# Kernel tuning notes

Measured on AMD Instinct MI355X. Metric: run time of the kernel, lower is better.

The kernel has to match this reference:

```python
import jax, jax.numpy as jnp
import numpy as np

N_WIN, P, K, PAD, M_SEL, B_SZ, C, DH = 2048, 64, 48, 8, 1536, 8, 128, 32
INNER = (C * 4 * 2 // 3 // 32) * 32  # gated GLU inner dim = 320


def _ln(x, g, b, eps=1e-5):
    m = x.mean(-1, keepdims=True)
    v = ((x - m) ** 2).mean(-1, keepdims=True)
    return (x - m) * jax.lax.rsqrt(v + eps) * g + b


def _forward(x, n1_g, n1_b, n2_g, n2_b, qkv_w, qkv_b, proj_w, proj_b,
             ls1_g, ls2_g, glu_w, glu_b, out_w, out_b,
             index_window, index_token, padding_index, asy_index, M, B, enable_CB):
    N, P_, C_ = x.shape
    H = C_ // DH
    scale = DH ** -0.5
    x = _ln(x, n1_g, n1_b)                              # norm1
    X = x                                               # (N, P, C) normalized copy
    XX = x[index_window].reshape(-1, C_)                # (M*P, C) gathered windows
    xn = XX.at[asy_index].set(_ln(XX[asy_index], n2_g, n2_b))
    shortcut = xn[asy_index]
    xt = xn[index_token].reshape(M, -1, C_)             # (M, K, C)
    Kt = xt.shape[1]
    qkv = (xt @ qkv_w + qkv_b).reshape(M, Kt, H, 3 * DH).transpose(0, 2, 1, 3)
    q, k, v = jnp.split(qkv, 3, axis=3)                 # each (M, H, K, DH)
    attn = jnp.einsum('mhqd,mhkd->mhqk', q, k) * scale  # (M, H, K, K)
    # scatter scores into dense per-token map keyed by KEY position, mask pads, gather back
    attn_map = jnp.zeros((XX.shape[0], Kt, H), attn.dtype)
    attn_map = attn_map.at[index_token].set(jnp.transpose(attn, (0, 3, 2, 1)).reshape(-1, Kt, H))
    attn_map = attn_map.at[padding_index].set(-10000.0)
    attn = jnp.transpose(attn_map[index_token].reshape(M, Kt, Kt, H), (0, 3, 2, 1))
    attn = jax.nn.softmax(attn, axis=-1)
    o = jnp.einsum('mhqk,mhkd->mqhd', attn, v).reshape(M, Kt, C_)
    o = o @ proj_w + proj_b
    XX = XX.at[index_token].set(o.reshape(-1, C_))
    xa = XX[asy_index]
    # sub-layers: ls1 -> residual -> norm2 -> mlp(+CB) -> ls2 -> residual
    xa = shortcut + xa * ls1_g
    shortcut = xa
    xa = _ln(xa, n2_g, n2_b)
    u, g = jnp.split(xa @ glu_w + glu_b, 2, axis=-1)
    xa = (u * jax.nn.gelu(g, approximate=False)) @ out_w + out_b
    if enable_CB:
        tXX = jnp.zeros_like(XX).at[asy_index].set(xa)
        tX = jnp.zeros_like(X).at[index_window].set(tXX.reshape(M, -1, C_))
        tX = tX.reshape(B, -1, C_)
        tX = 0.5 * tX + 0.5 * tX.mean(axis=1, keepdims=True)
        xa = tX.reshape(N, P_, C_)[index_window].reshape(-1, C_)[asy_index]
    xa = shortcut + xa * ls2_g
    XX = XX.at[asy_index].set(xa)
    XX = XX.at[padding_index].set(X[index_window].reshape(-1, C_)[padding_index])
    return X.at[index_window].set(XX.reshape(M, -1, C_))  # (N, P, C)


def setup_inputs() -> dict:
    key = jax.random.key(0)
    ks = jax.random.split(key, 6)
    rng = np.random.default_rng(0)
    index_window = jnp.asarray(np.sort(rng.choice(N_WIN, M_SEL, replace=False)).astype(np.int64))
    base = np.arange(M_SEL)[:, None] * P + np.arange(K)[None, :]   # (M, K) flat token ids in [0, M*P)
    pad = np.zeros((M_SEL, K), dtype=bool)
    pad[:, K - PAD:] = True                                        # last PAD tokens of each window are padding
    index_token = jnp.asarray(base.reshape(-1).astype(np.int64))   # (M*K,)
    padding_index = jnp.asarray(base[pad].astype(np.int64))        # (M*PAD,)
    asy_index = jnp.asarray(base[~pad].astype(np.int64))           # (M*(K-PAD),)
    s = 0.02
    return {
        'x': jax.random.normal(ks[0], (N_WIN, P, C), jnp.float32),
        'n1_g': jnp.ones((C,), jnp.float32), 'n1_b': jnp.zeros((C,), jnp.float32),
        'n2_g': jnp.ones((C,), jnp.float32), 'n2_b': jnp.zeros((C,), jnp.float32),
        'qkv_w': jax.random.normal(ks[1], (C, 3 * C), jnp.float32) * s,
        'qkv_b': jnp.zeros((3 * C,), jnp.float32),
        'proj_w': jax.random.normal(ks[2], (C, C), jnp.float32) * s,
        'proj_b': jnp.zeros((C,), jnp.float32),
        'ls1_g': jnp.full((C,), 1e-5, jnp.float32), 'ls2_g': jnp.full((C,), 1e-5, jnp.float32),
        'glu_w': jax.random.normal(ks[3], (C, 2 * INNER), jnp.float32) * s,
        'glu_b': jnp.zeros((2 * INNER,), jnp.float32),
        'out_w': jax.random.normal(ks[4], (INNER, C), jnp.float32) * s,
        'out_b': jnp.zeros((C,), jnp.float32),
        'index_window': index_window, 'index_token': index_token,
        'padding_index': padding_index, 'asy_index': asy_index,
        'M': M_SEL, 'B': B_SZ, 'enable_CB': 1,
    }


def reference(x, n1_g, n1_b, n2_g, n2_b, qkv_w, qkv_b, proj_w, proj_b,
              ls1_g, ls2_g, glu_w, glu_b, out_w, out_b,
              index_window, index_token, padding_index, asy_index, M, B, enable_CB):
    return _forward(x, n1_g, n1_b, n2_g, n2_b, qkv_w, qkv_b, proj_w, proj_b,
                    ls1_g, ls2_g, glu_w, glu_b, out_w, out_b,
                    index_window, index_token, padding_index, asy_index, M, B, enable_CB)
```

## Files before the change

### kernel.cpp

```cpp
#include <hip/hip_runtime.h>
#include <math.h>

typedef unsigned short u16;
typedef unsigned int   u32;
typedef __attribute__((ext_vector_type(8))) short bf16x8;
typedef __attribute__((ext_vector_type(4))) float f32x4;

#define N_WIN 2048
#define PW    64
#define KA    40
#define MSEL  1536
#define CH    128
#define NH    4
#define GLUI  320
#define NTOK  (MSEL*KA)
#define RPC   16384

__device__ __forceinline__ u16 f2b(float f) {
    u32 u = __float_as_uint(f);
    return (u16)((u + 0x7FFFu + ((u >> 16) & 1u)) >> 16);
}
__device__ __forceinline__ float b2f(u16 v) { return __uint_as_float(((u32)v) << 16); }

__device__ __forceinline__ float fgelu(float g) {
    return g / (1.f + __expf(-1.702f * g));
}

__global__ __launch_bounds__(256) void k_cvt(const float* __restrict__ qkv_w,
                                             const float* __restrict__ proj_w,
                                             const float* __restrict__ glu_w,
                                             const float* __restrict__ out_w,
                                             const int* __restrict__ iw,
                                             u16* __restrict__ wq, u16* __restrict__ wp,
                                             u16* __restrict__ wg, u16* __restrict__ wo,
                                             float* __restrict__ csum,
                                             int* __restrict__ selidx) {
    int idx = blockIdx.x * 256 + threadIdx.x;
    if (idx < 49152) {
        int n = idx / 128, k = idx % 128;
        wq[idx] = f2b(qkv_w[k * 384 + n]);
    } else if (idx < 65536) {
        int i = idx - 49152, n = i / 128, k = i % 128;
        wp[i] = f2b(proj_w[k * 128 + n]);
    } else if (idx < 147456) {
        int i = idx - 65536, n = i / 128, k = i % 128;
        wg[i] = f2b(glu_w[k * 640 + n]);
    } else if (idx < 188416) {
        int i = idx - 147456, n = i / 320, k = i % 320;
        wo[i] = f2b(out_w[k * 128 + n]);
    } else if (idx < 188416 + 8 * CH) {
        csum[idx - 188416] = 0.f;
    } else if (idx < 188416 + 8 * CH + N_WIN) {
        int w_ = idx - (188416 + 8 * CH);
        int lo = 0, hi = MSEL - 1, m = -1;
        while (lo <= hi) {
            int mid = (lo + hi) >> 1;
            int vw = iw[mid];
            if (vw == w_) { m = mid; break; }
            if (vw < w_) lo = mid + 1; else hi = mid - 1;
        }
        selidx[w_] = m;
    }
}

__global__ __launch_bounds__(256) void k_ln1(const float* __restrict__ x,
                                             const float* __restrict__ g1,
                                             const float* __restrict__ b1,
                                             const float* __restrict__ g2,
                                             const float* __restrict__ b2,
                                             const int* __restrict__ selidx,
                                             float* __restrict__ out,
                                             u16* __restrict__ s1h) {
    int wave = threadIdx.x >> 6, lane = threadIdx.x & 63;
    long row = (long)blockIdx.x * 8 + wave * 2 + (lane >> 5);
    int col = (lane & 31) * 4;
    float4 v = *(const float4*)(x + row * CH + col);
    float s  = v.x + v.y + v.z + v.w;
    float s2 = v.x * v.x + v.y * v.y + v.z * v.z + v.w * v.w;
    #pragma unroll
    for (int o = 16; o; o >>= 1) { s += __shfl_xor(s, o); s2 += __shfl_xor(s2, o); }
    float mu = s * (1.f / CH), var = s2 * (1.f / CH) - mu * mu;
    float r = rsqrtf(var + 1e-5f);
    float4 gg = *(const float4*)(g1 + col);
    float4 bb = *(const float4*)(b1 + col);
    f32x4 o4;
    o4[0] = (v.x - mu) * r * gg.x + bb.x;
    o4[1] = (v.y - mu) * r * gg.y + bb.y;
    o4[2] = (v.z - mu) * r * gg.z + bb.z;
    o4[3] = (v.w - mu) * r * gg.w + bb.w;

    int w_ = (int)(row >> 6), k_ = (int)(row & 63);
    int m = selidx[w_];
    bool overwritten = (m >= 0) && (k_ < KA);
    if (!overwritten) {
        __builtin_nontemporal_store(o4, (f32x4*)(out + row * CH + col));
    } else {
        float t  = o4[0] + o4[1] + o4[2] + o4[3];
        float t2 = o4[0] * o4[0] + o4[1] * o4[1] + o4[2] * o4[2] + o4[3] * o4[3];
        #pragma unroll
        for (int o = 16; o; o >>= 1) { t += __shfl_xor(t, o); t2 += __shfl_xor(t2, o); }
        float mu2 = t * (1.f / CH), var2 = t2 * (1.f / CH) - mu2 * mu2;
        float r2 = rsqrtf(var2 + 1e-5f);
        float4 gg2 = *(const float4*)(g2 + col);
        float4 bb2 = *(const float4*)(b2 + col);
        ushort4 q;
        q.x = f2b((o4[0] - mu2) * r2 * gg2.x + bb2.x);
        q.y = f2b((o4[1] - mu2) * r2 * gg2.y + bb2.y);
        q.z = f2b((o4[2] - mu2) * r2 * gg2.z + bb2.z);
        q.w = f2b((o4[3] - mu2) * r2 * gg2.w + bb2.w);
        *(ushort4*)(s1h + ((long)m * KA + k_) * CH + col) = q;
    }
}

__global__ __launch_bounds__(256, 4) void k_qkv(const u16* __restrict__ A,
                                                const u16* __restrict__ wq,
                                                const float* __restrict__ qkv_b,
                                                u16* __restrict__ qkb,
                                                u16* __restrict__ vtb) {
    __shared__ u16 Al[128][128];
    int tid = threadIdx.x, wid = tid >> 6, lane = tid & 63;
    int l15 = lane & 15, lg = lane >> 4;
    long m0 = (long)blockIdx.x * 128;
    int c0 = blockIdx.y * 128 + wid * 32;
    int h = c0 / 96, wi0 = c0 % 96;
    #pragma unroll
    for (int ch = 0; ch < 8; ++ch) {
        int id = tid + ch * 256; int row = id >> 4, c8 = id & 15;
        *(bf16x8*)&Al[row][(c8 ^ (row & 7)) * 8] = *(const bf16x8*)&A[(m0 + row) * CH + c8 * 8];
    }
    bf16x8 bf[2][4];
    #pragma unroll
    for (int j = 0; j < 2; ++j)
        #pragma unroll
        for (int ks = 0; ks < 4; ++ks)
            bf[j][ks] = *(const bf16x8*)&wq[(long)(c0 + j * 16 + l15) * CH + ks * 32 + lg * 8];
    __syncthreads();
    if (wi0 < 64) {
        float bc[2][4];
        #pragma unroll
        for (int j = 0; j < 2; ++j)
            #pragma unroll
            for (int r = 0; r < 4; ++r) bc[j][r] = qkv_b[c0 + j * 16 + lg * 4 + r];
        #pragma unroll
        for (int st = 0; st < 8; ++st) {
            f32x4 acc[2] = {};
            #pragma unroll
            for (int ks = 0; ks < 4; ++ks) {
                bf16x8 af = *(const bf16x8*)&Al[st * 16 + l15][((ks * 4 + lg) ^ (l15 & 7)) * 8];
                acc[0] = __builtin_amdgcn_mfma_f32_16x16x32_bf16(bf[0][ks], af, acc[0], 0, 0, 0);
                acc[1] = __builtin_amdgcn_mfma_f32_16x16x32_bf16(bf[1][ks], af, acc[1], 0, 0, 0);
            }
            long row = m0 + st * 16 + l15;
            #pragma unroll
            for (int j = 0; j < 2; ++j) {
                ushort4 o;
                o.x = f2b(acc[j][0] + bc[j][0]);
                o.y = f2b(acc[j][1] + bc[j][1]);
                o.z = f2b(acc[j][2] + bc[j][2]);
                o.w = f2b(acc[j][3] + bc[j][3]);
                *(ushort4*)&qkb[row * 256 + h * 64 + wi0 + j * 16 + lg * 4] = o;
            }
        }
    } else {
        float bc[2];
        bc[0] = qkv_b[c0 + l15];
        bc[1] = qkv_b[c0 + 16 + l15];
        #pragma unroll
        for (int st = 0; st < 8; ++st) {
            f32x4 acc[2] = {};
            #pragma unroll
            for (int ks = 0; ks < 4; ++ks) {
                bf16x8 af = *(const bf16x8*)&Al[st * 16 + l15][((ks * 4 + lg) ^ (l15 & 7)) * 8];
                acc[0] = __builtin_amdgcn_mfma_f32_16x16x32_bf16(af, bf[0][ks], acc[0], 0, 0, 0);
                acc[1] = __builtin_amdgcn_mfma_f32_16x16x32_bf16(af, bf[1][ks], acc[1], 0, 0, 0);
            }
            long base = m0 + st * 16 + lg * 4;
            int mm = (int)(base / KA), key = (int)(base % KA);
            #pragma unroll
            for (int j = 0; j < 2; ++j) {
                int d = j * 16 + l15;
                ushort4 o;
                o.x = f2b(acc[j][0] + bc[j]);
                o.y = f2b(acc[j][1] + bc[j]);
                o.z = f2b(acc[j][2] + bc[j]);
                o.w = f2b(acc[j][3] + bc[j]);
                *(ushort4*)&vtb[(((long)mm * NH + h) * 32 + d) * KA + key] = o;
            }
        }
    }
}

__global__ __launch_bounds__(256) void k_attn(const u16* __restrict__ qkb,
                                              const u16* __restrict__ vtb,
                                              u16* __restrict__ obuf) {
    __shared__ u16 qk[KA][256];
    __shared__ u16 vT[NH][32][64];
    int m = blockIdx.x, tid = threadIdx.x;
    int h = tid >> 6, lane = tid & 63, l15 = lane & 15, lg = lane >> 4;

    for (int i = tid; i < KA * 32; i += 256) {
        int j = i >> 5, seg = i & 31;
        *(bf16x8*)&qk[j][(seg ^ (j & 7)) * 8] = *(const bf16x8*)&qkb[((long)m * KA + j) * 256 + seg * 8];
    }
    for (int i = tid; i < NH * 32 * 8; i += 256) {
        int hh = i >> 8, rem = i & 255, d = rem >> 3, c = rem & 7;
        bf16x8 v = {};
        if (c < 5) v = *(const bf16x8*)&vtb[(((long)m * NH + hh) * 32 + d) * KA + c * 8];
        *(bf16x8*)&vT[hh][d][(c ^ (d & 7)) * 8] = v;
    }
    __syncthreads();

    bf16x8 aq[3], bk[3];
    #pragma unroll
    for (int t = 0; t < 3; ++t) {
        int rr = t * 16 + l15; if (rr > KA - 1) rr = KA - 1;
        aq[t] = *(const bf16x8*)&qk[rr][((h * 8 + lg) ^ (rr & 7)) * 8];
        bk[t] = *(const bf16x8*)&qk[rr][((h * 8 + 4 + lg) ^ (rr & 7)) * 8];
    }
    f32x4 zero = {};
    f32x4 s[3][3];
    #pragma unroll
    for (int mi = 0; mi < 3; ++mi)
        #pragma unroll
        for (int ni = 0; ni < 3; ++ni)
            s[mi][ni] = __builtin_amdgcn_mfma_f32_16x16x32_bf16(aq[mi], bk[ni], zero, 0, 0, 0);

    const float scale = 0.17677669529663687f;
    float inv_[3][4];
    #pragma unroll
    for (int mi = 0; mi < 3; ++mi)
        #pragma unroll
        for (int r = 0; r < 4; ++r) {
            float v0 = s[mi][0][r] * scale;
            float v1 = s[mi][1][r] * scale;
            float v2 = (l15 >= 8) ? -1e30f : s[mi][2][r] * scale;
            float mx = fmaxf(fmaxf(v0, v1), v2);
            #pragma unroll
            for (int o = 1; o < 16; o <<= 1) mx = fmaxf(mx, __shfl_xor(mx, o));
            float e0 = __expf(v0 - mx), e1 = __expf(v1 - mx), e2 = __expf(v2 - mx);
            float sm = e0 + e1 + e2;
            #pragma unroll
            for (int o = 1; o < 16; o <<= 1) sm += __shfl_xor(sm, o);
            inv_[mi][r] = 1.f / sm;
            int row = mi * 16 + lg * 4 + r;
            if (row < KA) {
                int rx = row & 7, off = l15 & 7, sb = l15 >> 3;
                qk[row][(((h * 8 + 0 + sb) ^ rx) << 3) | off] = f2b(e0);
                qk[row][(((h * 8 + 2 + sb) ^ rx) << 3) | off] = f2b(e1);
                qk[row][(((h * 8 + 4 + sb) ^ rx) << 3) | off] = f2b(e2);
            }
        }

    f32x4 o[3][2] = {};
    #pragma unroll
    for (int ks = 0; ks < 2; ++ks) {
        bf16x8 pa[3], vb[2];
        #pragma unroll
        for (int mi = 0; mi < 3; ++mi) {
            int rp = mi * 16 + l15; if (rp > KA - 1) rp = KA - 1;
            pa[mi] = *(const bf16x8*)&qk[rp][((h * 8 + ks * 4 + lg) ^ (rp & 7)) * 8];
        }
        #pragma unroll
        for (int nf = 0; nf < 2; ++nf) {
            int dr = nf * 16 + l15;
            vb[nf] = *(const bf16x8*)&vT[h][dr][((ks * 4 + lg) ^ (dr & 7)) * 8];
        }
        #pragma unroll
        for (int mi = 0; mi < 3; ++mi)
            #pragma unroll
            for (int nf = 0; nf < 2; ++nf)
                o[mi][nf] = __builtin_amdgcn_mfma_f32_16x16x32_bf16(pa[mi], vb[nf], o[mi][nf], 0, 0, 0);
    }
    #pragma unroll
    for (int mi = 0; mi < 3; ++mi)
        #pragma unroll
        for (int nf = 0; nf < 2; ++nf)
            #pragma unroll
            for (int r = 0; r < 4; ++r) {
                int row4 = mi * 16 + lg * 4 + r;
                if (row4 < KA)
                    obuf[((long)m * KA + row4) * CH + h * 32 + nf * 16 + l15] =
                        f2b(o[mi][nf][r] * inv_[mi][r]);
            }
}

__global__ __launch_bounds__(256, 3) void k_proj(const u16* __restrict__ obuf,
                                                 const u16* __restrict__ wp,
                                                 const float* __restrict__ proj_b,
                                                 const u16* __restrict__ s1h,
                                                 const float* __restrict__ ls1,
                                                 const float* __restrict__ g2,
                                                 const float* __restrict__ b2,
                                                 u16* __restrict__ r1h,
                                                 u16* __restrict__ hbuf) {
    __shared__ u16 Al[64][128];
    __shared__ float ps[4][64], ps2[4][64];
    int tid = threadIdx.x, wid = tid >> 6, lane = tid & 63;
    int l15 = lane & 15, lg = lane >> 4;
    long m0 = (long)blockIdx.x * 64;
    bf16x8 bf[2][4];
    #pragma unroll
    for (int j = 0; j < 2; ++j)
        #pragma unroll
        for (int ks = 0; ks < 4; ++ks)
            bf[j][ks] = *(const bf16x8*)&wp[(long)(wid * 32 + j * 16 + l15) * CH + ks * 32 + lg * 8];
    #pragma unroll
    for (int ch = 0; ch < 4; ++ch) {
        int id = tid + ch * 256; int row = id >> 4, c8 = id & 15;
        *(bf16x8*)&Al[row][(c8 ^ (row & 7)) * 8] = *(const bf16x8*)&obuf[(m0 + row) * CH + c8 * 8];
    }
    __syncthreads();
    float vals[4][2][4];
    #pragma unroll
    for (int st = 0; st < 4; ++st) {
        bf16x8 af[4];
        #pragma unroll
        for (int ks = 0; ks < 4; ++ks)
            af[ks] = *(const bf16x8*)&Al[st * 16 + l15][((ks * 4 + lg) ^ (l15 & 7)) * 8];
        f32x4 acc[2] = {};
        #pragma unroll
        for (int ks = 0; ks < 4; ++ks)
            #pragma unroll
            for (int j = 0; j < 2; ++j)
                acc[j] = __builtin_amdgcn_mfma_f32_16x16x32_bf16(af[ks], bf[j][ks], acc[j], 0, 0, 0);
        #pragma unroll
        for (int r = 0; r < 4; ++r) {
            long row = m0 + st * 16 + lg * 4 + r;
            float s = 0.f, s2 = 0.f;
            #pragma unroll
            for (int j = 0; j < 2; ++j) {
                int col = wid * 32 + j * 16 + l15;
                float v = acc[j][r] + proj_b[col];
                v = b2f(s1h[row * CH + col]) + v * ls1[col];
                vals[st][j][r] = v; s += v; s2 += v * v;
            }
            #pragma unroll
            for (int msk = 1; msk < 16; msk <<= 1) { s += __shfl_xor(s, msk); s2 += __shfl_xor(s2, msk); }
            if (l15 == 0) {
                ps[wid][st * 16 + lg * 4 + r]  = s;
                ps2[wid][st * 16 + lg * 4 + r] = s2;
            }
        }
    }
    __syncthreads();
    #pragma unroll
    for (int st = 0; st < 4; ++st)
        #pragma unroll
        for (int r = 0; r < 4; ++r) {
            int rl = st * 16 + lg * 4 + r;
            long row = m0 + rl;
            float s  = ps[0][rl] + ps[1][rl] + ps[2][rl] + ps[3][rl];
            float s2 = ps2[0][rl] + ps2[1][rl] + ps2[2][rl] + ps2[3][rl];
            float mu = s * (1.f / CH), var = s2 * (1.f / CH) - mu * mu;
            float rr = rsqrtf(var + 1e-5f);
            #pragma unroll
            for (int j = 0; j < 2; ++j) {
                int col = wid * 32 + j * 16 + l15;
                float v = vals[st][j][r];
                r1h[row * CH + col]  = f2b(v);
                hbuf[row * CH + col] = f2b((v - mu) * rr * g2[col] + b2[col]);
            }
        }
}

__global__ __launch_bounds__(256, 4) void k_glu(const u16* __restrict__ hbuf,
                                                const u16* __restrict__ wg,
                                                const float* __restrict__ glu_b,
                                                u16* __restrict__ act) {
    __shared__ u16 Al[128][128];
    int tid = threadIdx.x, wid = tid >> 6, lane = tid & 63;
    int l15 = lane & 15, lg = lane >> 4;
    long m0 = (long)blockIdx.x * 128;
    int c0 = blockIdx.y * 64 + wid * 16;
    #pragma unroll
    for (int ch = 0; ch < 8; ++ch) {
        int id = tid + ch * 256; int row = id >> 4, c8 = id & 15;
        *(bf16x8*)&Al[row][(c8 ^ (row & 7)) * 8] = *(const bf16x8*)&hbuf[(m0 + row) * CH + c8 * 8];
    }
    bf16x8 bu[4], bg[4];
    #pragma unroll
    for (int ks = 0; ks < 4; ++ks) {
        bu[ks] = *(const bf16x8*)&wg[(long)(c0 + l15) * CH + ks * 32 + lg * 8];
        bg[ks] = *(const bf16x8*)&wg[(long)(c0 + GLUI + l15) * CH + ks * 32 + lg * 8];
    }
    float bu_[4], bg_[4];
    #pragma unroll
    for (int r = 0; r < 4; ++r) {
        bu_[r] = glu_b[c0 + lg * 4 + r];
        bg_[r] = glu_b[c0 + GLUI + lg * 4 + r];
    }
    __syncthreads();
    #pragma unroll
    for (int st = 0; st < 8; ++st) {
        f32x4 au = {}, ag = {};
        #pragma unroll
        for (int ks = 0; ks < 4; ++ks) {
            bf16x8 af = *(const bf16x8*)&Al[st * 16 + l15][((ks * 4 + lg) ^ (l15 & 7)) * 8];
            au = __builtin_amdgcn_mfma_f32_16x16x32_bf16(bu[ks], af, au, 0, 0, 0);
            ag = __builtin_amdgcn_mfma_f32_16x16x32_bf16(bg[ks], af, ag, 0, 0, 0);
        }
        long row = m0 + st * 16 + l15;
        ushort4 o;
        {
            float uu, gg;
            uu = au[0] + bu_[0]; gg = ag[0] + bg_[0]; o.x = f2b(uu * fgelu(gg));
            uu = au[1] + bu_[1]; gg = ag[1] + bg_[1]; o.y = f2b(uu * fgelu(gg));
            uu = au[2] + bu_[2]; gg = ag[2] + bg_[2]; o.z = f2b(uu * fgelu(gg));
            uu = au[3] + bu_[3]; gg = ag[3] + bg_[3]; o.w = f2b(uu * fgelu(gg));
        }
        *(ushort4*)&act[row * GLUI + c0 + lg * 4] = o;
    }
}

__global__ __launch_bounds__(256, 3) void k_out(const u16* __restrict__ act,
                                                const u16* __restrict__ wo,
                                                const float* __restrict__ out_b,
                                                u16* __restrict__ mlph) {
    __shared__ u16 Al[128][192];
    int tid = threadIdx.x, wid = tid >> 6, lane = tid & 63;
    int l15 = lane & 15, lg = lane >> 4;
    long m0 = (long)blockIdx.x * 128;
    f32x4 acc[2][8] = {};
    #pragma unroll
    for (int kc = 0; kc < 2; ++kc) {
        #pragma unroll
        for (int ch = 0; ch < 10; ++ch) {
            int id = tid + ch * 256; int row = id / 20, c8 = id % 20;
            *(bf16x8*)&Al[row][(c8 ^ (row & 7)) * 8] =
                *(const bf16x8*)&act[(m0 + row) * GLUI + kc * 160 + c8 * 8];
        }
        bf16x8 bo[2][5];
        #pragma unroll
        for (int j = 0; j < 2; ++j)
            #pragma unroll
            for (int ks = 0; ks < 5; ++ks)
                bo[j][ks] = *(const bf16x8*)&wo[(long)(wid * 32 + j * 16 + l15) * GLUI + kc * 160 + ks * 32 + lg * 8];
        __syncthreads();
        #pragma unroll
        for (int st = 0; st < 8; ++st)
            #pragma unroll
            for (int ks = 0; ks < 5; ++ks) {
                bf16x8 af = *(const bf16x8*)&Al[st * 16 + l15][((ks * 4 + lg) ^ (l15 & 7)) * 8];
                acc[0][st] = __builtin_amdgcn_mfma_f32_16x16x32_bf16(bo[0][ks], af, acc[0][st], 0, 0, 0);
                acc[1][st] = __builtin_amdgcn_mfma_f32_16x16x32_bf16(bo[1][ks], af, acc[1][st], 0, 0, 0);
            }
        __syncthreads();
    }
    float bc[2][4];
    #pragma unroll
    for (int j = 0; j < 2; ++j)
        #pragma unroll
        for (int r = 0; r < 4; ++r) bc[j][r] = out_b[wid * 32 + j * 16 + lg * 4 + r];
    #pragma unroll
    for (int st = 0; st < 8; ++st) {
        long row = m0 + st * 16 + l15;
        #pragma unroll
        for (int j = 0; j < 2; ++j) {
            ushort4 o;
            o.x = f2b(acc[j][st][0] + bc[j][0]);
            o.y = f2b(acc[j][st][1] + bc[j][1]);
            o.z = f2b(acc[j][st][2] + bc[j][2]);
            o.w = f2b(acc[j][st][3] + bc[j][3]);
            *(ushort4*)&mlph[row * CH + wid * 32 + j * 16 + lg * 4] = o;
        }
    }
}

__global__ __launch_bounds__(256) void k_csum(const u16* __restrict__ mlph,
                                              const int* __restrict__ iw,
                                              float* __restrict__ csum) {
    __shared__ float acc[8][CH];
    __shared__ int wcid[3];
    int tid = threadIdx.x, c8 = tid & 15, rg = tid >> 4;
    int base_w = blockIdx.x * 3;
    if (tid < 3) wcid[tid] = iw[base_w + tid] >> 8;
    for (int i = tid; i < 8 * CH; i += 256) ((float*)acc)[i] = 0.f;
    __syncthreads();

    long base_row = (long)base_w * KA;
    float sum[8] = {};
    int curcid = wcid[0];
    #pragma unroll
    for (int it = 0; it < 8; ++it) {
        int r = rg + 16 * it;
        if (r >= 120) break;
        int cid = wcid[r / 40];
        if (cid != curcid) {
            #pragma unroll
            for (int k = 0; k < 8; ++k)
                if (sum[k] != 0.f) atomicAdd(&acc[curcid & 7][c8 * 8 + k], sum[k]);
            #pragma unroll
            for (int k = 0; k < 8; ++k) sum[k] = 0.f;
            curcid = cid;
        }
        bf16x8 v = *(const bf16x8*)&mlph[(base_row + r) * CH + c8 * 8];
        #pragma unroll
        for (int k = 0; k < 8; ++k) sum[k] += b2f((u16)v[k]);
    }
    #pragma unroll
    for (int k = 0; k < 8; ++k)
        if (sum[k] != 0.f) atomicAdd(&acc[curcid & 7][c8 * 8 + k], sum[k]);
    __syncthreads();
    for (int i = tid; i < 8 * CH; i += 256) {
        float v = ((float*)acc)[i];
        if (v != 0.f) atomicAdd(&csum[i], v);
    }
}

__global__ __launch_bounds__(256) void k_final(const u16* __restrict__ r1h,
                                               const u16* __restrict__ mlph,
                                               const float* __restrict__ csum,
                                               const float* __restrict__ ls2,
                                               const int* __restrict__ iw,
                                               const int* __restrict__ ecb,
                                               float* __restrict__ out) {
    long idx8 = (long)blockIdx.x * 256 + threadIdx.x;
    long row = idx8 >> 4;
    int seg = (int)(idx8 & 15) * 8;
    int m = (int)(row / KA), k = (int)(row % KA);
    int w = iw[m];
    int cb = ecb[0];
    int cid = w >> 8;
    bf16x8 rv = *(const bf16x8*)&r1h[row * CH + seg];
    bf16x8 mv = *(const bf16x8*)&mlph[row * CH + seg];
    float* dst = out + ((long)(w * PW + k)) * CH + seg;
    f32x4 o0, o1;
    float ot[8];
    #pragma unroll
    for (int t = 0; t < 8; ++t) {
        float xa = b2f((u16)mv[t]);
        if (cb) xa = 0.5f * xa + (0.5f / RPC) * csum[cid * CH + seg + t];
        ot[t] = b2f((u16)rv[t]) + xa * ls2[seg + t];
    }
    o0[0] = ot[0]; o0[1] = ot[1]; o0[2] = ot[2]; o0[3] = ot[3];
    o1[0] = ot[4]; o1[1] = ot[5]; o1[2] = ot[6]; o1[3] = ot[7];
    __builtin_nontemporal_store(o0, (f32x4*)dst);
    __builtin_nontemporal_store(o1, (f32x4*)(dst + 4));
}

extern "C" void kernel_launch(void* const* d_in, const int* in_sizes, int n_in,
                              void* d_out, int out_size, void* d_ws, size_t ws_size,
                              hipStream_t stream) {
    const float* x      = (const float*)d_in[0];
    const float* n1g    = (const float*)d_in[1];
    const float* n1b    = (const float*)d_in[2];
    const float* n2g    = (const float*)d_in[3];
    const float* n2b    = (const float*)d_in[4];
    const float* qkv_w  = (const float*)d_in[5];
    const float* qkv_b  = (const float*)d_in[6];
    const float* proj_w = (const float*)d_in[7];
    const float* proj_b = (const float*)d_in[8];
    const float* ls1    = (const float*)d_in[9];
    const float* ls2    = (const float*)d_in[10];
    const float* glu_w  = (const float*)d_in[11];
    const float* glu_b  = (const float*)d_in[12];
    const float* out_w  = (const float*)d_in[13];
    const float* out_b  = (const float*)d_in[14];
    const int*   iw     = (const int*)d_in[15];
    const int*   ecb    = (const int*)d_in[21];
    float* out = (float*)d_out;

    char* w = (char*)d_ws;
    u16*   s1h  = (u16*)w;
    u16*   qkb  = (u16*)(w + 15728640);
    u16*   act  = qkb;
    u16*   vtb  = (u16*)(w + 47185920);
    u16*   obuf = (u16*)(w + 62914560);
    u16*   r1h  = (u16*)(w + 78643200);
    u16*   hbuf = (u16*)(w + 94371840);
    u16*   mlph = (u16*)(w + 110100480);
    u16*   wq   = (u16*)(w + 125829120);
    u16*   wp   = wq + 384 * 128;
    u16*   wg   = wp + 128 * 128;
    u16*   wo   = wg + 640 * 128;
    float* csum = (float*)(w + 126205952);
    int*   selidx = (int*)(w + 126210048);

    k_cvt<<<(188416 + 8 * CH + N_WIN + 255) / 256, 256, 0, stream>>>(
        qkv_w, proj_w, glu_w, out_w, iw, wq, wp, wg, wo, csum, selidx);

    k_ln1 <<<N_WIN * PW / 8, 256, 0, stream>>>(x, n1g, n1b, n2g, n2b, selidx, out, s1h);
    k_qkv <<<dim3(NTOK / 128, 3), 256, 0, stream>>>(s1h, wq, qkv_b, qkb, vtb);
    k_attn<<<MSEL, 256, 0, stream>>>(qkb, vtb, obuf);
    k_proj<<<NTOK / 64, 256, 0, stream>>>(obuf, wp, proj_b, s1h, ls1, n2g, n2b, r1h, hbuf);
    k_glu <<<dim3(NTOK / 128, 5), 256, 0, stream>>>(hbuf, wg, glu_b, act);
    k_out <<<NTOK / 128, 256, 0, stream>>>(act, wo, out_b, mlph);
    k_csum<<<MSEL / 3, 256, 0, stream>>>(mlph, iw, csum);
    k_final<<<(NTOK * CH / 8) / 256, 256, 0, stream>>>(r1h, mlph, csum, ls2, iw, ecb, out);
    (void)in_sizes; (void)n_in; (void)out_size; (void)ws_size;
}
```

Baseline: 168.7 us.

## Fuse output projection, residual and norm2 into attention kernel

```diff
diff --git a/kernel.cpp b/kernel.cpp
--- a/kernel.cpp
+++ b/kernel.cpp
@@ -192,11 +192,27 @@
 
 __global__ __launch_bounds__(256) void k_attn(const u16* __restrict__ qkb,
                                               const u16* __restrict__ vtb,
-                                              u16* __restrict__ obuf) {
+                                              const u16* __restrict__ wp,
+                                              const float* __restrict__ proj_b,
+                                              const u16* __restrict__ s1h,
+                                              const float* __restrict__ ls1,
+                                              const float* __restrict__ g2,
+                                              const float* __restrict__ b2,
+                                              u16* __restrict__ r1h,
+                                              u16* __restrict__ hbuf) {
     __shared__ u16 qk[KA][256];
     __shared__ u16 vT[NH][32][64];
+    __shared__ u16 olds[48][128];
+    __shared__ float ps[4][48], ps2[4][48];
     int m = blockIdx.x, tid = threadIdx.x;
     int h = tid >> 6, lane = tid & 63, l15 = lane & 15, lg = lane >> 4;
+
+    bf16x8 bfp[2][4];
+    #pragma unroll
+    for (int j = 0; j < 2; ++j)
+        #pragma unroll
+        for (int ks = 0; ks < 4; ++ks)
+            bfp[j][ks] = *(const bf16x8*)&wp[(long)(h * 32 + j * 16 + l15) * CH + ks * 32 + lg * 8];
 
     for (int i = tid; i < KA * 32; i += 256) {
         int j = i >> 5, seg = i & 31;
@@ -278,84 +294,65 @@
             #pragma unroll
             for (int r = 0; r < 4; ++r) {
                 int row4 = mi * 16 + lg * 4 + r;
-                if (row4 < KA)
-                    obuf[((long)m * KA + row4) * CH + h * 32 + nf * 16 + l15] =
+                if (row4 < KA) {
+                    int ci = h * 32 + nf * 16 + l15;
+                    olds[row4][(((ci >> 3) ^ (row4 & 7)) << 3) | (ci & 7)] =
                         f2b(o[mi][nf][r] * inv_[mi][r]);
-            }
-}
-
-__global__ __launch_bounds__(256, 3) void k_proj(const u16* __restrict__ obuf,
-                                                 const u16* __restrict__ wp,
-                                                 const float* __restrict__ proj_b,
-                                                 const u16* __restrict__ s1h,
-                                                 const float* __restrict__ ls1,
-                                                 const float* __restrict__ g2,
-                                                 const float* __restrict__ b2,
-                                                 u16* __restrict__ r1h,
-                                                 u16* __restrict__ hbuf) {
-    __shared__ u16 Al[64][128];
-    __shared__ float ps[4][64], ps2[4][64];
-    int tid = threadIdx.x, wid = tid >> 6, lane = tid & 63;
-    int l15 = lane & 15, lg = lane >> 4;
-    long m0 = (long)blockIdx.x * 64;
-    bf16x8 bf[2][4];
-    #pragma unroll
-    for (int j = 0; j < 2; ++j)
+                }
+            }
+    __syncthreads();
+
+    float vals[3][2][4];
+    #pragma unroll
+    for (int st = 0; st < 3; ++st) {
+        bf16x8 af[4];
+        int rr = st * 16 + l15;
         #pragma unroll
         for (int ks = 0; ks < 4; ++ks)
-            bf[j][ks] = *(const bf16x8*)&wp[(long)(wid * 32 + j * 16 + l15) * CH + ks * 32 + lg * 8];
-    #pragma unroll
-    for (int ch = 0; ch < 4; ++ch) {
-        int id = tid + ch * 256; int row = id >> 4, c8 = id & 15;
-        *(bf16x8*)&Al[row][(c8 ^ (row & 7)) * 8] = *(const bf16x8*)&obuf[(m0 + row) * CH + c8 * 8];
-    }
-    __syncthreads();
-    float vals[4][2][4];
-    #pragma unroll
-    for (int st = 0; st < 4; ++st) {
-        bf16x8 af[4];
+            af[ks] = *(const bf16x8*)&olds[rr][((ks * 4 + lg) ^ (rr & 7)) * 8];
+        f32x4 acc[2] = {};
         #pragma unroll
         for (int ks = 0; ks < 4; ++ks)
-            af[ks] = *(const bf16x8*)&Al[st * 16 + l15][((ks * 4 + lg) ^ (l15 & 7)) * 8];
-        f32x4 acc[2] = {};
-        #pragma unroll
-        for (int ks = 0; ks < 4; ++ks)
             #pragma unroll
             for (int j = 0; j < 2; ++j)
-                acc[j] = __builtin_amdgcn_mfma_f32_16x16x32_bf16(af[ks], bf[j][ks], acc[j], 0, 0, 0);
+                acc[j] = __builtin_amdgcn_mfma_f32_16x16x32_bf16(af[ks], bfp[j][ks], acc[j], 0, 0, 0);
         #pragma unroll
         for (int r = 0; r < 4; ++r) {
-            long row = m0 + st * 16 + lg * 4 + r;
-            float s = 0.f, s2 = 0.f;
+            int rowl = st * 16 + lg * 4 + r;
+            float sl = 0.f, sl2 = 0.f;
+            if (rowl < KA) {
+                long row = (long)m * KA + rowl;
+                #pragma unroll
+                for (int j = 0; j < 2; ++j) {
+                    int col = h * 32 + j * 16 + l15;
+                    float v = acc[j][r] + proj_b[col];
+                    v = b2f(s1h[row * CH + col]) + v * ls1[col];
+                    vals[st][j][r] = v; sl += v; sl2 += v * v;
+                }
+            }
+            #pragma unroll
+            for (int msk = 1; msk < 16; msk <<= 1) { sl += __shfl_xor(sl, msk); sl2 += __shfl_xor(sl2, msk); }
+            if (l15 == 0 && rowl < KA) {
+                ps[h][rowl]  = sl;
+                ps2[h][rowl] = sl2;
+            }
+        }
+    }
+    __syncthreads();
+    #pragma unroll
+    for (int st = 0; st < 3; ++st)
+        #pragma unroll
+        for (int r = 0; r < 4; ++r) {
+            int rowl = st * 16 + lg * 4 + r;
+            if (rowl >= KA) continue;
+            long row = (long)m * KA + rowl;
+            float sl  = ps[0][rowl] + ps[1][rowl] + ps[2][rowl] + ps[3][rowl];
+            float sl2 = ps2[0][rowl] + ps2[1][rowl] + ps2[2][rowl] + ps2[3][rowl];
+            float mu = sl * (1.f / CH), var = sl2 * (1.f / CH) - mu * mu;
+            float rr = rsqrtf(var + 1e-5f);
             #pragma unroll
             for (int j = 0; j < 2; ++j) {
-                int col = wid * 32 + j * 16 + l15;
-                float v = acc[j][r] + proj_b[col];
-                v = b2f(s1h[row * CH + col]) + v * ls1[col];
-                vals[st][j][r] = v; s += v; s2 += v * v;
-            }
-            #pragma unroll
-            for (int msk = 1; msk < 16; msk <<= 1) { s += __shfl_xor(s, msk); s2 += __shfl_xor(s2, msk); }
-            if (l15 == 0) {
-                ps[wid][st * 16 + lg * 4 + r]  = s;
-                ps2[wid][st * 16 + lg * 4 + r] = s2;
-            }
-        }
-    }
-    __syncthreads();
-    #pragma unroll
-    for (int st = 0; st < 4; ++st)
-        #pragma unroll
-        for (int r = 0; r < 4; ++r) {
-            int rl = st * 16 + lg * 4 + r;
-            long row = m0 + rl;
-            float s  = ps[0][rl] + ps[1][rl] + ps[2][rl] + ps[3][rl];
-            float s2 = ps2[0][rl] + ps2[1][rl] + ps2[2][rl] + ps2[3][rl];
-            float mu = s * (1.f / CH), var = s2 * (1.f / CH) - mu * mu;
-            float rr = rsqrtf(var + 1e-5f);
-            #pragma unroll
-            for (int j = 0; j < 2; ++j) {
-                int col = wid * 32 + j * 16 + l15;
+                int col = h * 32 + j * 16 + l15;
                 float v = vals[st][j][r];
                 r1h[row * CH + col]  = f2b(v);
                 hbuf[row * CH + col] = f2b((v - mu) * rr * g2[col] + b2[col]);
@@ -565,7 +562,6 @@
     u16*   qkb  = (u16*)(w + 15728640);
     u16*   act  = qkb;
     u16*   vtb  = (u16*)(w + 47185920);
-    u16*   obuf = (u16*)(w + 62914560);
     u16*   r1h  = (u16*)(w + 78643200);
     u16*   hbuf = (u16*)(w + 94371840);
     u16*   mlph = (u16*)(w + 110100480);
@@ -581,8 +577,7 @@
 
     k_ln1 <<<N_WIN * PW / 8, 256, 0, stream>>>(x, n1g, n1b, n2g, n2b, selidx, out, s1h);
     k_qkv <<<dim3(NTOK / 128, 3), 256, 0, stream>>>(s1h, wq, qkv_b, qkb, vtb);
-    k_attn<<<MSEL, 256, 0, stream>>>(qkb, vtb, obuf);
-    k_proj<<<NTOK / 64, 256, 0, stream>>>(obuf, wp, proj_b, s1h, ls1, n2g, n2b, r1h, hbuf);
+    k_attn<<<MSEL, 256, 0, stream>>>(qkb, vtb, wp, proj_b, s1h, ls1, n2g, n2b, r1h, hbuf);
     k_glu <<<dim3(NTOK / 128, 5), 256, 0, stream>>>(hbuf, wg, glu_b, act);
     k_out <<<NTOK / 128, 256, 0, stream>>>(act, wo, out_b, mlph);
     k_csum<<<MSEL / 3, 256, 0, stream>>>(mlph, iw, csum);
```

Result: no change. 170.4 us (+1.0%).
